# Kernel optimization log

Measured on AMD Instinct MI355X. Metric: run time of the kernel, lower is better.

Reference implementation:

```python
import jax, jax.numpy as jnp
import numpy as np

B, S = 128, 200
Q, K, V, C, SUM = 20000, 128, 128, 64, 128


def setup_inputs() -> dict:
    key = jax.random.key(0)
    ks = jax.random.split(key, 14)
    stdev = 1.0 / np.sqrt(C + K)  # NTM-style memory init bound

    def lin_w(k, fan_in, shape):
        b = 1.0 / np.sqrt(fan_in)
        return jax.random.uniform(k, shape, jnp.float32, -b, b)

    # embeddings with padding_idx=0 zeroed (PAD_INDEX=0)
    q_emb = jax.random.normal(ks[0], (Q + 1, K), jnp.float32).at[0].set(0.0)
    i_emb = jax.random.normal(ks[1], (2 * Q + 1, V), jnp.float32).at[0].set(0.0)
    key_memory = jax.random.uniform(ks[2], (K, C), jnp.float32, -stdev, stdev)
    init_value_memory = jax.random.uniform(ks[3], (V, C), jnp.float32, -stdev, stdev)
    erase_W = lin_w(ks[4], V, (V, V))
    erase_b = lin_w(ks[5], V, (V,))
    add_W = lin_w(ks[6], V, (V, V))
    add_b = lin_w(ks[7], V, (V,))
    summ_W = lin_w(ks[8], V + K, (V + K, SUM))
    summ_b = lin_w(ks[9], V + K, (SUM,))
    out_W = lin_w(ks[10], SUM, (SUM, 1))
    out_b = lin_w(ks[11], SUM, (1,))
    inp = jax.random.randint(ks[12], (B, S), 0, 2 * Q + 1)
    target_id = jax.random.randint(ks[13], (B,), 0, Q + 1)
    return dict(q_emb=q_emb, i_emb=i_emb, key_memory=key_memory,
                init_value_memory=init_value_memory,
                erase_W=erase_W, erase_b=erase_b, add_W=add_W, add_b=add_b,
                summ_W=summ_W, summ_b=summ_b, out_W=out_W, out_b=out_b,
                input=inp, target_id=target_id)


def reference(q_emb, i_emb, key_memory, init_value_memory,
              erase_W, erase_b, add_W, add_b,
              summ_W, summ_b, out_W, out_b,
              input, target_id):
    Qn = q_emb.shape[0] - 1
    bsz = input.shape[0]
    # map interaction index -> question id
    qid = input - Qn * (input > Qn).astype(input.dtype)          # (B,S)
    # all per-step quantities are independent of memory state -> precompute
    iv = i_emb[input]                                            # (B,S,V)
    e = jax.nn.sigmoid(iv @ erase_W + erase_b)                   # (B,S,V)
    a = jnp.tanh(iv @ add_W + add_b)                             # (B,S,V)
    w = jax.nn.softmax(q_emb[qid] @ key_memory, axis=-1)         # (B,S,C)

    mem0 = jnp.broadcast_to(init_value_memory, (bsz,) + init_value_memory.shape)  # (B,V,C)

    def step(mem, xs):
        e_t, a_t, w_t = xs                                       # (B,V),(B,V),(B,C)
        erase = e_t[:, :, None] * w_t[:, None, :]                # rank-1 outer, (B,V,C)
        add = a_t[:, :, None] * w_t[:, None, :]
        mem = mem * (1.0 - erase) + add
        return mem, None

    xs = (jnp.swapaxes(e, 0, 1), jnp.swapaxes(a, 0, 1), jnp.swapaxes(w, 0, 1))
    mem, _ = jax.lax.scan(step, mem0, xs)                        # (B,V,C)

    qv = q_emb[target_id]                                        # (B,K)
    wt = jax.nn.softmax(qv @ key_memory, axis=-1)                # (B,C)
    read = jnp.einsum('bvc,bc->bv', mem, wt)                     # (B,V)
    summ = jnp.tanh(jnp.concatenate([read, qv], axis=-1) @ summ_W + summ_b)
    return summ @ out_W + out_b                                  # (B,1), pre-sigmoid
```

## Files before the change

kernel.cpp:

```cpp
#include <hip/hip_runtime.h>
#include <hip/hip_bf16.h>
#include <hip/hip_fp16.h>

#define B_ 128
#define S_ 200
#define QN_ 20000
#define V_ 128
#define K_ 128
#define C_ 64
#define SUM_ 128
#define NCH 4
#define CL 50
#define RP 52

using short8 = __attribute__((ext_vector_type(8))) short;
using f32x4  = __attribute__((ext_vector_type(4))) float;

__device__ __forceinline__ float fast_sigmoid(float x) { return 1.f / (1.f + __expf(-x)); }
__device__ __forceinline__ float fast_tanh(float x)    { return 1.f - 2.f / (__expf(2.f * x) + 1.f); }

template<bool BF>
__device__ __forceinline__ float ld(const void* p, long long i) {
    if (BF) return __bfloat162float(((const __hip_bfloat16*)p)[i]);
    return ((const float*)p)[i];
}

__device__ __forceinline__ unsigned short f2bf(float v) {
    __hip_bfloat16 h = __float2bfloat16(v);
    unsigned short u;
    __builtin_memcpy(&u, &h, 2);
    return u;
}

__device__ __forceinline__ void ld4h(const __half* p, float* out) {
    const float2 f01 = __half22float2(*(const __half2*)p);
    const float2 f23 = __half22float2(*(const __half2*)(p + 2));
    out[0] = f01.x; out[1] = f01.y; out[2] = f23.x; out[3] = f23.y;
}

__device__ __forceinline__ int probe_flag_wave(const void* erase_b) {
    const unsigned* w = (const unsigned*)erase_b;
    const int lane = threadIdx.x & 63;
    const unsigned lo = w[lane] & 0xffffu;
    const float f = __uint_as_float(lo << 16);
    const unsigned long long bal = __ballot(!(fabsf(f) <= 0.5f));
    return (__popcll(bal) <= 8) ? 1 : 0;
}

template<bool BF>
__device__ __forceinline__ void wt_body(
    const void* q_emb, const void* key_memory, const int* __restrict__ target_id,
    int b, float* __restrict__ wt_buf)
{
    const int t = threadIdx.x;
    if (t >= 64) return;
    const long long qrow = (long long)target_id[b] * K_;
    float logit = 0.f;
    #pragma unroll 8
    for (int i = 0; i < K_; ++i)
        logit += ld<BF>(q_emb, qrow + i) * ld<BF>(key_memory, i * C_ + t);
    float m = logit;
    for (int off = 32; off > 0; off >>= 1)
        m = fmaxf(m, __shfl_xor(m, off, 64));
    const float ex = __expf(logit - m);
    float ssum = ex;
    for (int off = 32; off > 0; off >>= 1)
        ssum += __shfl_xor(ssum, off, 64);
    wt_buf[b * C_ + t] = ex / ssum;
}

__global__ __launch_bounds__(256) void dkvmn_prepack(
    const void* erase_W, const void* add_W, const void* key_memory,
    const void* erase_b, const void* q_emb, const int* __restrict__ target_id,
    unsigned short* __restrict__ wpack, float* __restrict__ wt_buf)
{
    const int bf = probe_flag_wave(erase_b);
    if (blockIdx.x >= 20) {
        const int b = blockIdx.x - 20;
        if (bf) wt_body<true>(q_emb, key_memory, target_id, b, wt_buf);
        else    wt_body<false>(q_emb, key_memory, target_id, b, wt_buf);
        return;
    }
    const int fid = blockIdx.x * 256 + threadIdx.x;
    if (fid >= 5120) return;
    const int lane = fid & 63;
    const int ks = (fid >> 6) & 3;
    const int wv = (fid >> 8) & 3;
    const int q  = fid >> 10;
    const int nt = wv + 4 * q;
    const void* Wsrc;
    int ncol, ldn;
    if (q < 2)      { Wsrc = erase_W;    ncol = nt * 16 + (lane & 15);        ldn = 128; }
    else if (q < 4) { Wsrc = add_W;      ncol = (nt - 8) * 16 + (lane & 15);  ldn = 128; }
    else            { Wsrc = key_memory; ncol = (nt - 16) * 16 + (lane & 15); ldn = 64; }
    const int k8 = (lane >> 4) * 8;
    unsigned short o[8];
    #pragma unroll
    for (int jj = 0; jj < 8; ++jj) {
        const long long idx = (long long)(ks * 32 + k8 + jj) * ldn + ncol;
        const float v = bf ? ld<true>(Wsrc, idx) : ld<false>(Wsrc, idx);
        o[jj] = f2bf(v);
    }
    *(uint4*)(wpack + (size_t)fid * 8) = *(const uint4*)o;
}

struct FusedLDS {
    unsigned short ivA[RP * 136];
    unsigned short qvA[RP * 136];
    __half esh[RP * 136];
    __half ash[RP * 136];
    float  wlog[RP * 68];
    int sidx[RP], sqid[RP];
};

template<bool BF>
__device__ __forceinline__ void fused_body(
    const void* q_emb, const void* i_emb,
    const void* erase_b, const void* add_b,
    const int* __restrict__ input, const unsigned short* __restrict__ wpack,
    __half2* __restrict__ du, FusedLDS& sm)
{
    const int bid = blockIdx.x;
    const int b = bid & 127;
    const int chunk = bid >> 7;
    const int t = threadIdx.x;
    const int wv = t >> 6;
    const int lane = t & 63;
    const int lrow = lane & 15;
    const int lk8 = (lane >> 4) * 8;

    if (t < RP) {
        const int s = (t < CL) ? t : 0;
        const int ix = input[b * S_ + chunk * CL + s];
        sm.sidx[t] = ix;
        sm.sqid[t] = ix > QN_ ? ix - QN_ : ix;
    }
    __syncthreads();

    #pragma unroll
    for (int r = 0; r < 7; ++r) {
        const int j = t + 256 * r;
        if (j < 2 * RP * 16) {
            const int tensor = j >= RP * 16;
            const int jj = j - tensor * (RP * 16);
            const int row = jj >> 4;
            const int seg = jj & 15;
            const int gr = tensor ? sm.sqid[row] : sm.sidx[row];
            unsigned short* dst = (tensor ? sm.qvA : sm.ivA) + row * 136 + seg * 8;
            if (BF) {
                const unsigned short* src = (const unsigned short*)(tensor ? q_emb : i_emb);
                *(uint4*)dst = *(const uint4*)(src + (long long)gr * 128 + seg * 8);
            } else {
                const float* src = (const float*)(tensor ? q_emb : i_emb) + (long long)gr * 128 + seg * 8;
                const float4 f0 = *(const float4*)src;
                const float4 f1 = *(const float4*)(src + 4);
                unsigned short o[8] = {f2bf(f0.x), f2bf(f0.y), f2bf(f0.z), f2bf(f0.w),
                                       f2bf(f1.x), f2bf(f1.y), f2bf(f1.z), f2bf(f1.w)};
                *(uint4*)dst = *(const uint4*)o;
            }
        }
    }

    short8 bfr[5][4];
    int nco[5];
    float biasq[4];
    #pragma unroll
    for (int q = 0; q < 5; ++q) {
        const int nt = wv + 4 * q;
        if (q < 2)      nco[q] = nt * 16 + lrow;
        else if (q < 4) nco[q] = (nt - 8) * 16 + lrow;
        else            nco[q] = (nt - 16) * 16 + lrow;
        if (q < 2)      biasq[q] = ld<BF>(erase_b, nco[q]);
        else if (q < 4) biasq[q] = ld<BF>(add_b, nco[q]);
        #pragma unroll
        for (int ks = 0; ks < 4; ++ks)
            bfr[q][ks] = *(const short8*)(wpack +
                ((size_t)(((q * 4 + wv) * 4 + ks) * 64 + lane)) * 8);
    }
    __syncthreads();

    #pragma unroll
    for (int mt = 0; mt < 4; ++mt) {
        short8 afr[4];
        const unsigned short* ar = sm.ivA + (mt * 16 + lrow) * 136 + lk8;
        #pragma unroll
        for (int ks = 0; ks < 4; ++ks)
            afr[ks] = *(const short8*)(ar + ks * 32);
        #pragma unroll
        for (int q = 0; q < 4; ++q) {
            f32x4 acc = {0.f, 0.f, 0.f, 0.f};
            #pragma unroll
            for (int ks = 0; ks < 4; ++ks)
                acc = __builtin_amdgcn_mfma_f32_16x16x32_bf16(afr[ks], bfr[q][ks], acc, 0, 0, 0);
            const int ncol = nco[q];
            const float bb = biasq[q];
            #pragma unroll
            for (int r = 0; r < 4; ++r) {
                const int orow = mt * 16 + (lane >> 4) * 4 + r;
                if (orow < CL) {
                    const float y = acc[r] + bb;
                    if (q < 2) sm.esh[orow * 136 + ncol] = __float2half(fast_sigmoid(y));
                    else       sm.ash[orow * 136 + ncol] = __float2half(fast_tanh(y));
                }
            }
        }
    }
    #pragma unroll
    for (int mt = 0; mt < 4; ++mt) {
        short8 afr[4];
        const unsigned short* ar = sm.qvA + (mt * 16 + lrow) * 136 + lk8;
        #pragma unroll
        for (int ks = 0; ks < 4; ++ks)
            afr[ks] = *(const short8*)(ar + ks * 32);
        f32x4 acc = {0.f, 0.f, 0.f, 0.f};
        #pragma unroll
        for (int ks = 0; ks < 4; ++ks)
            acc = __builtin_amdgcn_mfma_f32_16x16x32_bf16(afr[ks], bfr[4][ks], acc, 0, 0, 0);
        #pragma unroll
        for (int r = 0; r < 4; ++r) {
            const int orow = mt * 16 + (lane >> 4) * 4 + r;
            if (orow < CL)
                sm.wlog[orow * 68 + nco[4]] = acc[r];
        }
    }
    __syncthreads();

    #pragma unroll
    for (int pass = 0; pass < 2; ++pass) {
        const int row = pass * 32 + (t >> 3);
        if (row < CL) {
            const int cs = t & 7;
            float* wr = &sm.wlog[row * 68 + cs * 8];
            float v[8];
            *(float4*)&v[0] = *(const float4*)&wr[0];
            *(float4*)&v[4] = *(const float4*)&wr[4];
            float m = v[0];
            #pragma unroll
            for (int ii = 1; ii < 8; ++ii) m = fmaxf(m, v[ii]);
            m = fmaxf(m, __shfl_xor(m, 1, 64));
            m = fmaxf(m, __shfl_xor(m, 2, 64));
            m = fmaxf(m, __shfl_xor(m, 4, 64));
            float s = 0.f;
            #pragma unroll
            for (int ii = 0; ii < 8; ++ii) { v[ii] = __expf(v[ii] - m); s += v[ii]; }
            s += __shfl_xor(s, 1, 64);
            s += __shfl_xor(s, 2, 64);
            s += __shfl_xor(s, 4, 64);
            const float inv = 1.f / s;
            *(float4*)&wr[0] = make_float4(v[0]*inv, v[1]*inv, v[2]*inv, v[3]*inv);
            *(float4*)&wr[4] = make_float4(v[4]*inv, v[5]*inv, v[6]*inv, v[7]*inv);
        }
    }
    __syncthreads();

    const int vg = t >> 3;
    const int cg = t & 7;
    const int v0 = vg * 4, c0 = cg * 8;

    float ym[4][8], Dm[4][8];
    #pragma unroll
    for (int i = 0; i < 4; ++i)
        #pragma unroll
        for (int j = 0; j < 8; ++j) { ym[i][j] = 0.f; Dm[i][j] = 1.f; }

    for (int s = 0; s < CL; ++s) {
        float ev[4], av[4], wv8[8];
        ld4h(sm.esh + s * 136 + v0, ev);
        ld4h(sm.ash + s * 136 + v0, av);
        *(float4*)&wv8[0] = *(const float4*)(sm.wlog + s * 68 + c0);
        *(float4*)&wv8[4] = *(const float4*)(sm.wlog + s * 68 + c0 + 4);
        #pragma unroll
        for (int i = 0; i < 4; ++i) {
            #pragma unroll
            for (int j = 0; j < 8; ++j) {
                const float d = fmaf(-ev[i], wv8[j], 1.f);
                Dm[i][j] *= d;
                ym[i][j] = fmaf(d, ym[i][j], av[i] * wv8[j]);
            }
        }
    }

    __half2* dbase = du + ((size_t)(chunk * B_ + b) * (V_ * C_));
    #pragma unroll
    for (int i = 0; i < 4; ++i) {
        __half2 h[8];
        #pragma unroll
        for (int j = 0; j < 8; ++j)
            h[j] = __floats2half2_rn(Dm[i][j], ym[i][j]);
        __half2* dst = dbase + (v0 + i) * C_ + c0;
        *(uint4*)dst = *(const uint4*)&h[0];
        *(uint4*)(dst + 4) = *(const uint4*)&h[4];
    }
}

__global__ __launch_bounds__(256) void dkvmn_fused(
    const void* q_emb, const void* i_emb,
    const void* erase_b, const void* add_b,
    const int* __restrict__ input, const unsigned short* __restrict__ wpack,
    __half2* __restrict__ du)
{
    __shared__ FusedLDS sm;
    if (probe_flag_wave(erase_b))
        fused_body<true>(q_emb, i_emb, erase_b, add_b, input, wpack, du, sm);
    else
        fused_body<false>(q_emb, i_emb, erase_b, add_b, input, wpack, du, sm);
}

template<bool BF>
__device__ __forceinline__ void foldfinal_body(
    const void* init_value_memory, const void* q_emb,
    const void* summ_W, const void* summ_b,
    const void* out_W, const void* out_b,
    const int* __restrict__ target_id,
    const __half2* __restrict__ du, const float* __restrict__ wt_buf,
    void* __restrict__ outp, float* readl, float* summl)
{
    const int b = blockIdx.x;
    const int t = threadIdx.x;
    const int cg = t & 7;
    const int c0 = cg * 8;

    float wt8[8];
    *(float4*)&wt8[0] = *(const float4*)(wt_buf + b * C_ + c0);
    *(float4*)&wt8[4] = *(const float4*)(wt_buf + b * C_ + c0 + 4);

    #pragma unroll
    for (int sub = 0; sub < 4; ++sub) {
        const int v = sub * 32 + (t >> 3);

        uint4 qa[NCH], qb[NCH];
        #pragma unroll
        for (int ch = 0; ch < NCH; ++ch) {
            const __half2* base = du + ((size_t)(ch * B_ + b) * (V_ * C_)) + v * C_ + c0;
            qa[ch] = *(const uint4*)base;
            qb[ch] = *(const uint4*)(base + 4);
        }

        float mem[8];
        #pragma unroll
        for (int k = 0; k < 8; ++k)
            mem[k] = ld<BF>(init_value_memory, v * C_ + c0 + k);

        #pragma unroll
        for (int ch = 0; ch < NCH; ++ch) {
            const __half2* hA = (const __half2*)&qa[ch];
            const __half2* hB = (const __half2*)&qb[ch];
            #pragma unroll
            for (int k = 0; k < 4; ++k) {
                const float2 fA = __half22float2(hA[k]);
                mem[k] = fmaf(fA.x, mem[k], fA.y);
                const float2 fB = __half22float2(hB[k]);
                mem[4 + k] = fmaf(fB.x, mem[4 + k], fB.y);
            }
        }

        float pacc = 0.f;
        #pragma unroll
        for (int k = 0; k < 8; ++k) pacc += mem[k] * wt8[k];
        pacc += __shfl_xor(pacc, 1, 64);
        pacc += __shfl_xor(pacc, 2, 64);
        pacc += __shfl_xor(pacc, 4, 64);
        if (cg == 0) readl[v] = pacc;
    }
    __syncthreads();

    if (t < SUM_) {
        const long long qrow = (long long)target_id[b] * K_;
        float acc = ld<BF>(summ_b, t);
        #pragma unroll 8
        for (int i = 0; i < 128; ++i)
            acc += readl[i] * ld<BF>(summ_W, i * SUM_ + t);
        #pragma unroll 8
        for (int i = 0; i < 128; ++i)
            acc += ld<BF>(q_emb, qrow + i) * ld<BF>(summ_W, (128 + i) * SUM_ + t);
        summl[t] = fast_tanh(acc);
    }
    __syncthreads();

    if (t < 64) {
        float oacc = summl[t] * ld<BF>(out_W, t) + summl[t + 64] * ld<BF>(out_W, t + 64);
        for (int off = 32; off > 0; off >>= 1)
            oacc += __shfl_xor(oacc, off, 64);
        if (t == 0) {
            const float res = oacc + ld<BF>(out_b, 0);
            if (BF) ((__hip_bfloat16*)outp)[b] = __float2bfloat16(res);
            else    ((float*)outp)[b] = res;
        }
    }
}

__global__ __launch_bounds__(256) void dkvmn_foldfinal(
    const void* init_value_memory, const void* q_emb,
    const void* summ_W, const void* summ_b,
    const void* out_W, const void* out_b, const void* erase_b,
    const int* __restrict__ target_id,
    const __half2* __restrict__ du, const float* __restrict__ wt_buf,
    void* __restrict__ outp)
{
    __shared__ float readl[V_], summl[SUM_];
    if (probe_flag_wave(erase_b))
        foldfinal_body<true>(init_value_memory, q_emb, summ_W, summ_b, out_W, out_b,
                             target_id, du, wt_buf, outp, readl, summl);
    else
        foldfinal_body<false>(init_value_memory, q_emb, summ_W, summ_b, out_W, out_b,
                              target_id, du, wt_buf, outp, readl, summl);
}

extern "C" void kernel_launch(void* const* d_in, const int* in_sizes, int n_in,
                              void* d_out, int out_size, void* d_ws, size_t ws_size,
                              hipStream_t stream) {
    const void* q_emb             = d_in[0];
    const void* i_emb             = d_in[1];
    const void* key_memory        = d_in[2];
    const void* init_value_memory = d_in[3];
    const void* erase_W           = d_in[4];
    const void* erase_b           = d_in[5];
    const void* add_W             = d_in[6];
    const void* add_b             = d_in[7];
    const void* summ_W            = d_in[8];
    const void* summ_b            = d_in[9];
    const void* out_W             = d_in[10];
    const void* out_b             = d_in[11];
    const int* input     = (const int*)d_in[12];
    const int* target_id = (const int*)d_in[13];

    unsigned short* wpack = (unsigned short*)d_ws;
    __half2* du = (__half2*)(wpack + 5120 * 8);
    float* wt_buf = (float*)(du + (size_t)NCH * B_ * V_ * C_);

    dkvmn_prepack<<<148, 256, 0, stream>>>(
        erase_W, add_W, key_memory, erase_b, q_emb, target_id, wpack, wt_buf);
    dkvmn_fused<<<NCH * B_, 256, 0, stream>>>(
        q_emb, i_emb, erase_b, add_b, input, wpack, du);
    dkvmn_foldfinal<<<B_, 256, 0, stream>>>(
        init_value_memory, q_emb, summ_W, summ_b, out_W, out_b, erase_b,
        target_id, du, wt_buf, d_out);
}
```

Measured before the change: 145.8 us.

## Remove prepack kernel; load weights in fused kernel and compute wt in foldfinal

Drops the separate prepack launch. Each fused block now reads erase_W, add_W and key_memory directly with strided scalar loads and converts them to bf16 MFMA fragments itself. The target-attention softmax moves into the foldfinal kernel's first wave and is kept in LDS. This saves one kernel launch and the workspace round trip, at the cost of 512 blocks each doing redundant uncoalesced weight loads and conversions.

```diff
diff --git a/kernel.cpp b/kernel.cpp
--- a/kernel.cpp
+++ b/kernel.cpp
@@ -47,63 +47,6 @@
     return (__popcll(bal) <= 8) ? 1 : 0;
 }
 
-template<bool BF>
-__device__ __forceinline__ void wt_body(
-    const void* q_emb, const void* key_memory, const int* __restrict__ target_id,
-    int b, float* __restrict__ wt_buf)
-{
-    const int t = threadIdx.x;
-    if (t >= 64) return;
-    const long long qrow = (long long)target_id[b] * K_;
-    float logit = 0.f;
-    #pragma unroll 8
-    for (int i = 0; i < K_; ++i)
-        logit += ld<BF>(q_emb, qrow + i) * ld<BF>(key_memory, i * C_ + t);
-    float m = logit;
-    for (int off = 32; off > 0; off >>= 1)
-        m = fmaxf(m, __shfl_xor(m, off, 64));
-    const float ex = __expf(logit - m);
-    float ssum = ex;
-    for (int off = 32; off > 0; off >>= 1)
-        ssum += __shfl_xor(ssum, off, 64);
-    wt_buf[b * C_ + t] = ex / ssum;
-}
-
-__global__ __launch_bounds__(256) void dkvmn_prepack(
-    const void* erase_W, const void* add_W, const void* key_memory,
-    const void* erase_b, const void* q_emb, const int* __restrict__ target_id,
-    unsigned short* __restrict__ wpack, float* __restrict__ wt_buf)
-{
-    const int bf = probe_flag_wave(erase_b);
-    if (blockIdx.x >= 20) {
-        const int b = blockIdx.x - 20;
-        if (bf) wt_body<true>(q_emb, key_memory, target_id, b, wt_buf);
-        else    wt_body<false>(q_emb, key_memory, target_id, b, wt_buf);
-        return;
-    }
-    const int fid = blockIdx.x * 256 + threadIdx.x;
-    if (fid >= 5120) return;
-    const int lane = fid & 63;
-    const int ks = (fid >> 6) & 3;
-    const int wv = (fid >> 8) & 3;
-    const int q  = fid >> 10;
-    const int nt = wv + 4 * q;
-    const void* Wsrc;
-    int ncol, ldn;
-    if (q < 2)      { Wsrc = erase_W;    ncol = nt * 16 + (lane & 15);        ldn = 128; }
-    else if (q < 4) { Wsrc = add_W;      ncol = (nt - 8) * 16 + (lane & 15);  ldn = 128; }
-    else            { Wsrc = key_memory; ncol = (nt - 16) * 16 + (lane & 15); ldn = 64; }
-    const int k8 = (lane >> 4) * 8;
-    unsigned short o[8];
-    #pragma unroll
-    for (int jj = 0; jj < 8; ++jj) {
-        const long long idx = (long long)(ks * 32 + k8 + jj) * ldn + ncol;
-        const float v = bf ? ld<true>(Wsrc, idx) : ld<false>(Wsrc, idx);
-        o[jj] = f2bf(v);
-    }
-    *(uint4*)(wpack + (size_t)fid * 8) = *(const uint4*)o;
-}
-
 struct FusedLDS {
     unsigned short ivA[RP * 136];
     unsigned short qvA[RP * 136];
@@ -116,8 +59,9 @@
 template<bool BF>
 __device__ __forceinline__ void fused_body(
     const void* q_emb, const void* i_emb,
+    const void* erase_W, const void* add_W, const void* key_memory,
     const void* erase_b, const void* add_b,
-    const int* __restrict__ input, const unsigned short* __restrict__ wpack,
+    const int* __restrict__ input,
     __half2* __restrict__ du, FusedLDS& sm)
 {
     const int bid = blockIdx.x;
@@ -167,15 +111,23 @@
     #pragma unroll
     for (int q = 0; q < 5; ++q) {
         const int nt = wv + 4 * q;
-        if (q < 2)      nco[q] = nt * 16 + lrow;
-        else if (q < 4) nco[q] = (nt - 8) * 16 + lrow;
-        else            nco[q] = (nt - 16) * 16 + lrow;
+        const void* Wsrc;
+        int ldn;
+        if (q < 2)      { Wsrc = erase_W;    nco[q] = nt * 16 + lrow;        ldn = 128; }
+        else if (q < 4) { Wsrc = add_W;      nco[q] = (nt - 8) * 16 + lrow;  ldn = 128; }
+        else            { Wsrc = key_memory; nco[q] = (nt - 16) * 16 + lrow; ldn = 64; }
         if (q < 2)      biasq[q] = ld<BF>(erase_b, nco[q]);
         else if (q < 4) biasq[q] = ld<BF>(add_b, nco[q]);
         #pragma unroll
-        for (int ks = 0; ks < 4; ++ks)
-            bfr[q][ks] = *(const short8*)(wpack +
-                ((size_t)(((q * 4 + wv) * 4 + ks) * 64 + lane)) * 8);
+        for (int ks = 0; ks < 4; ++ks) {
+            unsigned short o[8];
+            #pragma unroll
+            for (int jj = 0; jj < 8; ++jj) {
+                const long long idx = (long long)(ks * 32 + lk8 + jj) * ldn + nco[q];
+                o[jj] = f2bf(ld<BF>(Wsrc, idx));
+            }
+            bfr[q][ks] = *(const short8*)o;
+        }
     }
     __syncthreads();
 
@@ -295,34 +247,54 @@
 
 __global__ __launch_bounds__(256) void dkvmn_fused(
     const void* q_emb, const void* i_emb,
+    const void* erase_W, const void* add_W, const void* key_memory,
     const void* erase_b, const void* add_b,
-    const int* __restrict__ input, const unsigned short* __restrict__ wpack,
+    const int* __restrict__ input,
     __half2* __restrict__ du)
 {
     __shared__ FusedLDS sm;
     if (probe_flag_wave(erase_b))
-        fused_body<true>(q_emb, i_emb, erase_b, add_b, input, wpack, du, sm);
+        fused_body<true>(q_emb, i_emb, erase_W, add_W, key_memory,
+                         erase_b, add_b, input, du, sm);
     else
-        fused_body<false>(q_emb, i_emb, erase_b, add_b, input, wpack, du, sm);
+        fused_body<false>(q_emb, i_emb, erase_W, add_W, key_memory,
+                          erase_b, add_b, input, du, sm);
 }
 
 template<bool BF>
 __device__ __forceinline__ void foldfinal_body(
-    const void* init_value_memory, const void* q_emb,
+    const void* init_value_memory, const void* q_emb, const void* key_memory,
     const void* summ_W, const void* summ_b,
     const void* out_W, const void* out_b,
     const int* __restrict__ target_id,
-    const __half2* __restrict__ du, const float* __restrict__ wt_buf,
-    void* __restrict__ outp, float* readl, float* summl)
+    const __half2* __restrict__ du,
+    void* __restrict__ outp, float* wtl, float* readl, float* summl)
 {
     const int b = blockIdx.x;
     const int t = threadIdx.x;
     const int cg = t & 7;
     const int c0 = cg * 8;
 
+    if (t < 64) {
+        const long long qrow = (long long)target_id[b] * K_;
+        float logit = 0.f;
+        #pragma unroll 8
+        for (int i = 0; i < K_; ++i)
+            logit += ld<BF>(q_emb, qrow + i) * ld<BF>(key_memory, i * C_ + t);
+        float m = logit;
+        for (int off = 32; off > 0; off >>= 1)
+            m = fmaxf(m, __shfl_xor(m, off, 64));
+        const float ex = __expf(logit - m);
+        float ssum = ex;
+        for (int off = 32; off > 0; off >>= 1)
+            ssum += __shfl_xor(ssum, off, 64);
+        wtl[t] = ex / ssum;
+    }
+    __syncthreads();
+
     float wt8[8];
-    *(float4*)&wt8[0] = *(const float4*)(wt_buf + b * C_ + c0);
-    *(float4*)&wt8[4] = *(const float4*)(wt_buf + b * C_ + c0 + 4);
+    *(float4*)&wt8[0] = *(const float4*)(wtl + c0);
+    *(float4*)&wt8[4] = *(const float4*)(wtl + c0 + 4);
 
     #pragma unroll
     for (int sub = 0; sub < 4; ++sub) {
@@ -390,20 +362,20 @@
 }
 
 __global__ __launch_bounds__(256) void dkvmn_foldfinal(
-    const void* init_value_memory, const void* q_emb,
+    const void* init_value_memory, const void* q_emb, const void* key_memory,
     const void* summ_W, const void* summ_b,
     const void* out_W, const void* out_b, const void* erase_b,
     const int* __restrict__ target_id,
-    const __half2* __restrict__ du, const float* __restrict__ wt_buf,
+    const __half2* __restrict__ du,
     void* __restrict__ outp)
 {
-    __shared__ float readl[V_], summl[SUM_];
+    __shared__ float wtl[C_], readl[V_], summl[SUM_];
     if (probe_flag_wave(erase_b))
-        foldfinal_body<true>(init_value_memory, q_emb, summ_W, summ_b, out_W, out_b,
-                             target_id, du, wt_buf, outp, readl, summl);
+        foldfinal_body<true>(init_value_memory, q_emb, key_memory, summ_W, summ_b,
+                             out_W, out_b, target_id, du, outp, wtl, readl, summl);
     else
-        foldfinal_body<false>(init_value_memory, q_emb, summ_W, summ_b, out_W, out_b,
-                              target_id, du, wt_buf, outp, readl, summl);
+        foldfinal_body<false>(init_value_memory, q_emb, key_memory, summ_W, summ_b,
+                              out_W, out_b, target_id, du, outp, wtl, readl, summl);
 }
 
 extern "C" void kernel_launch(void* const* d_in, const int* in_sizes, int n_in,
@@ -424,15 +396,11 @@
     const int* input     = (const int*)d_in[12];
     const int* target_id = (const int*)d_in[13];
 
-    unsigned short* wpack = (unsigned short*)d_ws;
-    __half2* du = (__half2*)(wpack + 5120 * 8);
-    float* wt_buf = (float*)(du + (size_t)NCH * B_ * V_ * C_);
-
-    dkvmn_prepack<<<148, 256, 0, stream>>>(
-        erase_W, add_W, key_memory, erase_b, q_emb, target_id, wpack, wt_buf);
+    __half2* du = (__half2*)d_ws;
+
     dkvmn_fused<<<NCH * B_, 256, 0, stream>>>(
-        q_emb, i_emb, erase_b, add_b, input, wpack, du);
+        q_emb, i_emb, erase_W, add_W, key_memory, erase_b, add_b, input, du);
     dkvmn_foldfinal<<<B_, 256, 0, stream>>>(
-        init_value_memory, q_emb, summ_W, summ_b, out_W, out_b, erase_b,
-        target_id, du, wt_buf, d_out);
-}
+        init_value_memory, q_emb, key_memory, summ_W, summ_b, out_W, out_b,
+        erase_b, target_id, du, d_out);
+}
```

Measured after the change: 143.1 us. Within noise of the previous version (-1.8%).
